# Kernel optimization log

Hardware: AMD Instinct MI355X
Metric: run time of the kernel (lower is better)

Reference implementation:

```python
import jax, jax.numpy as jnp
import numpy as np

B, S, D, H = 2, 2048, 1024, 16
DH = D // H  # 64


def setup_inputs() -> dict:
    key = jax.random.key(0)
    ks = jax.random.split(key, 6)
    scale = 1.0 / np.sqrt(D)
    x = jax.random.normal(ks[0], (B, S, D), dtype=jnp.float32)
    Wq = jax.random.normal(ks[1], (D, D), dtype=jnp.float32) * scale
    Wk = jax.random.normal(ks[2], (D, D), dtype=jnp.float32) * scale
    Wv = jax.random.normal(ks[3], (D, D), dtype=jnp.float32) * scale
    Wo = jax.random.normal(ks[4], (D, D), dtype=jnp.float32) * scale
    zeros = jnp.zeros((D,), dtype=jnp.float32)
    return {"x": x, "Wq": Wq, "bq": zeros, "Wk": Wk, "bk": zeros,
            "Wv": Wv, "bv": zeros, "Wo": Wo, "bo": zeros}


def reference(x, Wq, bq, Wk, bk, Wv, bv, Wo, bo):
    # x: [B, S, D]
    def split_heads(t):
        # [B, S, D] -> [B, H, S, DH]
        return t.reshape(B, S, H, DH).transpose(0, 2, 1, 3)

    q = split_heads(x @ Wq + bq)
    k = split_heads(x @ Wk + bk)
    v = split_heads(x @ Wv + bv)

    scores = jnp.einsum('bhqd,bhkd->bhqk', q, k) / jnp.sqrt(jnp.float32(DH))
    weights = jax.nn.softmax(scores, axis=-1)          # [B, H, S, S]
    o = jnp.einsum('bhqk,bhkd->bhqd', weights, v)       # [B, H, S, DH]
    o = o.transpose(0, 2, 1, 3).reshape(B, S, D)        # merge heads
    return o @ Wo + bo
```

## Files before the change

kernel.cpp:

```cpp
#include <hip/hip_runtime.h>
#include <hip/hip_bf16.h>

#define DEV __device__ __forceinline__

typedef short bf16x8 __attribute__((ext_vector_type(8)));
typedef float f32x4 __attribute__((ext_vector_type(4)));
typedef unsigned int u32;

constexpr int BB = 2, SS = 2048, DD = 1024, HH = 16, DHD = 64;
constexpr int MM = BB * SS;
#define QSC 0.1803368801111f

#if __has_builtin(__builtin_amdgcn_exp2f)
#define EXP2(x) __builtin_amdgcn_exp2f(x)
#else
#define EXP2(x) exp2f(x)
#endif

DEV unsigned short f2bf(float f) {
    union { float f; unsigned int u; } v; v.f = f;
    return (unsigned short)((v.u + 0x8000u) >> 16);
}
DEV u32 pk2bf(float a, float b) {
    union { float f; u32 u; } ua, ub; ua.f = a; ub.f = b;
    return ((ua.u + 0x8000u) >> 16) | ((ub.u + 0x8000u) & 0xffff0000u);
}

DEV bf16x8 ld_bf16x8(const unsigned short* p) { return *(const bf16x8*)p; }

DEV void gl16(const unsigned short* g, unsigned short* l) {
    __builtin_amdgcn_global_load_lds(
        (const __attribute__((address_space(1))) u32*)g,
        (__attribute__((address_space(3))) u32*)l, 16, 0, 0);
}

__global__ void x2bf(const float* __restrict__ x, unsigned short* __restrict__ xb) {
    int i = blockIdx.x * 256 + threadIdx.x;
    float4 v = ((const float4*)x)[i];
    uint2 o;
    o.x = pk2bf(v.x, v.y);
    o.y = pk2bf(v.z, v.w);
    ((uint2*)xb)[i] = o;
}

__global__ void transpose_w4(const float* __restrict__ W0, const float* __restrict__ W1,
                             const float* __restrict__ W2, const float* __restrict__ W3,
                             unsigned short* __restrict__ WtBase) {
    __shared__ float tile[32][33];
    const float* W = (blockIdx.z == 0) ? W0 : (blockIdx.z == 1) ? W1 : (blockIdx.z == 2) ? W2 : W3;
    unsigned short* Wt = WtBase + (size_t)blockIdx.z * DD * DD;
    int n0 = blockIdx.x * 32, k0 = blockIdx.y * 32;
    int tx = threadIdx.x, ty = threadIdx.y;
    #pragma unroll
    for (int i = 0; i < 4; ++i)
        tile[ty + 8 * i][tx] = W[(size_t)(k0 + ty + 8 * i) * DD + n0 + tx];
    __syncthreads();
    #pragma unroll
    for (int i = 0; i < 4; ++i)
        Wt[(size_t)(n0 + ty + 8 * i) * DD + k0 + tx] = f2bf(tile[tx][ty + 8 * i]);
}

__global__ __launch_bounds__(256) void qkv_gemm(
    const unsigned short* __restrict__ xb,
    const unsigned short* __restrict__ WtBase,
    const float* __restrict__ bq, const float* __restrict__ bk, const float* __restrict__ bv,
    unsigned short* __restrict__ Qb, unsigned short* __restrict__ Kb, unsigned short* __restrict__ Vt)
{
    __shared__ __align__(16) unsigned short Ald[2][128 * 32];
    __shared__ __align__(16) unsigned short Bld[2][128 * 32];

    const int z = blockIdx.z;
    const unsigned short* Wt = WtBase + (size_t)z * DD * DD;
    const float* bias = (z == 0) ? bq : (z == 1) ? bk : bv;

    const int m0g = blockIdx.y * 128;
    const int n0g = blockIdx.x * 128;
    const int wave = threadIdx.x >> 6, lane = threadIdx.x & 63;
    const int quad = lane >> 4, lcol = lane & 15;
    const int mb = (wave & 1) * 64, nb = (wave >> 1) * 64;

    f32x4 acc[4][4];
    #pragma unroll
    for (int i = 0; i < 4; ++i)
        #pragma unroll
        for (int j = 0; j < 4; ++j) acc[i][j] = (f32x4){0.f, 0.f, 0.f, 0.f};

    auto stage = [&](int ks, int bf) {
        #pragma unroll
        for (int i = 0; i < 4; ++i) {
            int j = wave * 4 + i;
            if (j < 8) {
                int bi = j * 64 + lane;
                int row = bi >> 2, p = (bi & 3) ^ (row & 3);
                gl16(xb + (size_t)(m0g + row) * DD + ks + p * 8, &Ald[bf][j * 512]);
            } else {
                int jj = j - 8;
                int bi = jj * 64 + lane;
                int row = bi >> 2, p = (bi & 3) ^ (row & 3);
                gl16(Wt + (size_t)(n0g + row) * DD + ks + p * 8, &Bld[bf][jj * 512]);
            }
        }
    };

    stage(0, 0);
    __syncthreads();

    for (int kk = 0; kk < 32; ++kk) {
        int bf = kk & 1;
        if (kk + 1 < 32) stage((kk + 1) * 32, (kk + 1) & 1);
        bf16x8 af[4], bfr[4];
        #pragma unroll
        for (int mt = 0; mt < 4; ++mt) {
            int row = mb + mt * 16 + lcol;
            af[mt] = ld_bf16x8(&Ald[bf][(row * 4 + (quad ^ (row & 3))) * 8]);
        }
        #pragma unroll
        for (int nt = 0; nt < 4; ++nt) {
            int row = nb + nt * 16 + lcol;
            bfr[nt] = ld_bf16x8(&Bld[bf][(row * 4 + (quad ^ (row & 3))) * 8]);
        }
        if (z < 2) {
            #pragma unroll
            for (int mt = 0; mt < 4; ++mt)
                #pragma unroll
                for (int nt = 0; nt < 4; ++nt)
                    acc[mt][nt] = __builtin_amdgcn_mfma_f32_16x16x32_bf16(bfr[nt], af[mt], acc[mt][nt], 0, 0, 0);
        } else {
            #pragma unroll
            for (int mt = 0; mt < 4; ++mt)
                #pragma unroll
                for (int nt = 0; nt < 4; ++nt)
                    acc[mt][nt] = __builtin_amdgcn_mfma_f32_16x16x32_bf16(af[mt], bfr[nt], acc[mt][nt], 0, 0, 0);
        }
        __syncthreads();
    }

    if (z < 2) {
        unsigned short* dst = (z == 0) ? Qb : Kb;
        const float sc = (z == 0) ? QSC : 1.0f;
        #pragma unroll
        for (int mt = 0; mt < 4; ++mt)
            #pragma unroll
            for (int nt = 0; nt < 4; ++nt) {
                int m = m0g + mb + mt * 16 + lcol;
                int nbt = n0g + nb + nt * 16 + quad * 4;
                int b = m >> 11, s = m & (SS - 1);
                int h = nbt >> 6, dh0 = nbt & 63;
                float4 bv4 = *(const float4*)&bias[nbt];
                uint2 o;
                o.x = pk2bf((acc[mt][nt][0] + bv4.x) * sc, (acc[mt][nt][1] + bv4.y) * sc);
                o.y = pk2bf((acc[mt][nt][2] + bv4.z) * sc, (acc[mt][nt][3] + bv4.w) * sc);
                *(uint2*)&dst[(((size_t)b * HH + h) * SS + s) * DHD + dh0] = o;
            }
    } else {
        #pragma unroll
        for (int mt = 0; mt < 4; ++mt)
            #pragma unroll
            for (int nt = 0; nt < 4; ++nt) {
                int n = n0g + nb + nt * 16 + lcol;
                int mbt = m0g + mb + mt * 16 + quad * 4;
                int h = n >> 6, dh = n & 63;
                int b = mbt >> 11, s0 = mbt & (SS - 1);
                float bvv = bias[n];
                uint2 o;
                o.x = pk2bf(acc[mt][nt][0] + bvv, acc[mt][nt][1] + bvv);
                o.y = pk2bf(acc[mt][nt][2] + bvv, acc[mt][nt][3] + bvv);
                *(uint2*)&Vt[(((size_t)b * HH + h) * DHD + dh) * SS + s0] = o;
            }
    }
}

__global__ __launch_bounds__(256) void attn(
    const unsigned short* __restrict__ Qb,
    const unsigned short* __restrict__ Kb,
    const unsigned short* __restrict__ Vt,
    unsigned short* __restrict__ Ob)
{
    __shared__ __align__(16) unsigned short Kld[2][64 * 64];
    __shared__ __align__(16) unsigned short Vld[2][64 * 64];
    __shared__ __align__(16) unsigned short tb[4][2][16 * 72];

    const int qt = blockIdx.x;
    const int bh = blockIdx.y;
    const int b = bh >> 4, h = bh & (HH - 1);
    const unsigned short* Qbh = Qb + (size_t)bh * SS * DHD;
    const unsigned short* Kbh = Kb + (size_t)bh * SS * DHD;
    const unsigned short* Vbh = Vt + (size_t)bh * DHD * SS;

    const int wave = threadIdx.x >> 6, lane = threadIdx.x & 63;
    const int quad = lane >> 4, lcol = lane & 15;
    const int rowbase = qt * 128 + wave * 32;

    bf16x8 qf[2][2];
    #pragma unroll
    for (int mt = 0; mt < 2; ++mt)
        #pragma unroll
        for (int kf = 0; kf < 2; ++kf)
            qf[mt][kf] = ld_bf16x8(Qbh + (size_t)(rowbase + mt * 16 + lcol) * DHD + kf * 32 + quad * 8);

    auto stage = [&](int c, int bf) {
        int kb = c * 64;
        #pragma unroll
        for (int i = 0; i < 4; ++i) {
            int j = wave * 4 + i;
            if (j < 8) {
                int bi = j * 64 + lane;
                int r = bi >> 3, p = (bi & 7) ^ (r & 7);
                gl16(Kbh + (size_t)(kb + r) * DHD + p * 8, &Kld[bf][j * 512]);
            } else {
                int jj = j - 8;
                int bi = jj * 64 + lane;
                int dh = bi >> 3, p = (bi & 7) ^ (dh & 7);
                gl16(Vbh + (size_t)dh * SS + kb + p * 8, &Vld[bf][jj * 512]);
            }
        }
    };

    stage(0, 0);
    __syncthreads();

    float m0 = -1e30f;
    #pragma unroll
    for (int kt = 0; kt < 4; ++kt) {
        int r0 = kt * 16 + lcol;
        bf16x8 ka0 = ld_bf16x8(&Kld[0][(r0 * 8 + (quad ^ (r0 & 7))) * 8]);
        bf16x8 ka1 = ld_bf16x8(&Kld[0][(r0 * 8 + ((quad + 4) ^ (r0 & 7))) * 8]);
        #pragma unroll
        for (int mt = 0; mt < 2; ++mt) {
            f32x4 s = (f32x4){0.f, 0.f, 0.f, 0.f};
            s = __builtin_amdgcn_mfma_f32_16x16x32_bf16(ka0, qf[mt][0], s, 0, 0, 0);
            s = __builtin_amdgcn_mfma_f32_16x16x32_bf16(ka1, qf[mt][1], s, 0, 0, 0);
            #pragma unroll
            for (int r = 0; r < 4; ++r) m0 = fmaxf(m0, s[r]);
        }
    }
    #pragma unroll
    for (int msk = 1; msk < 64; msk <<= 1) m0 = fmaxf(m0, __shfl_xor(m0, msk, 64));

    f32x4 oacc[2][4];
    #pragma unroll
    for (int mt = 0; mt < 2; ++mt)
        #pragma unroll
        for (int nt = 0; nt < 4; ++nt) oacc[mt][nt] = (f32x4){0.f, 0.f, 0.f, 0.f};
    float ps[2] = {0.f, 0.f};

    for (int c = 0; c < 32; ++c) {
        int bf = c & 1;
        if (c + 1 < 32) stage(c + 1, (c + 1) & 1);

        #pragma unroll
        for (int kt = 0; kt < 4; ++kt) {
            int r0 = kt * 16 + lcol;
            bf16x8 ka0 = ld_bf16x8(&Kld[bf][(r0 * 8 + (quad ^ (r0 & 7))) * 8]);
            bf16x8 ka1 = ld_bf16x8(&Kld[bf][(r0 * 8 + ((quad + 4) ^ (r0 & 7))) * 8]);
            #pragma unroll
            for (int mt = 0; mt < 2; ++mt) {
                f32x4 s = (f32x4){0.f, 0.f, 0.f, 0.f};
                s = __builtin_amdgcn_mfma_f32_16x16x32_bf16(ka0, qf[mt][0], s, 0, 0, 0);
                s = __builtin_amdgcn_mfma_f32_16x16x32_bf16(ka1, qf[mt][1], s, 0, 0, 0);
                float e0 = EXP2(s[0] - m0), e1 = EXP2(s[1] - m0);
                float e2 = EXP2(s[2] - m0), e3 = EXP2(s[3] - m0);
                ps[mt] += (e0 + e1) + (e2 + e3);
                *(uint2*)&tb[wave][mt][lcol * 72 + kt * 16 + quad * 4] =
                    make_uint2(pk2bf(e0, e1), pk2bf(e2, e3));
            }
        }

        #pragma unroll
        for (int kf2 = 0; kf2 < 2; ++kf2) {
            bf16x8 vb[4];
            #pragma unroll
            for (int nt = 0; nt < 4; ++nt) {
                int dh = nt * 16 + lcol;
                vb[nt] = ld_bf16x8(&Vld[bf][(dh * 8 + ((kf2 * 4 + quad) ^ (dh & 7))) * 8]);
            }
            #pragma unroll
            for (int mt = 0; mt < 2; ++mt) {
                bf16x8 pa = *(const bf16x8*)&tb[wave][mt][lcol * 72 + kf2 * 32 + quad * 8];
                #pragma unroll
                for (int nt = 0; nt < 4; ++nt)
                    oacc[mt][nt] = __builtin_amdgcn_mfma_f32_16x16x32_bf16(pa, vb[nt], oacc[mt][nt], 0, 0, 0);
            }
        }
        __syncthreads();
    }

    #pragma unroll
    for (int mt = 0; mt < 2; ++mt) {
        ps[mt] += __shfl_xor(ps[mt], 16, 64);
        ps[mt] += __shfl_xor(ps[mt], 32, 64);
    }
    float inv[2] = {1.0f / ps[0], 1.0f / ps[1]};
    #pragma unroll
    for (int mt = 0; mt < 2; ++mt)
        #pragma unroll
        for (int r = 0; r < 4; ++r) {
            float iv = __shfl(inv[mt], quad * 4 + r, 64);
            int srow = rowbase + mt * 16 + quad * 4 + r;
            size_t base = (((size_t)b * SS + srow) * HH + h) * DHD;
            #pragma unroll
            for (int nt = 0; nt < 4; ++nt)
                Ob[base + nt * 16 + lcol] = f2bf(oacc[mt][nt][r] * iv);
        }
}

__global__ __launch_bounds__(256) void out_gemm(
    const unsigned short* __restrict__ Ob,
    const unsigned short* __restrict__ Wto,
    const float* __restrict__ bo,
    float* __restrict__ out)
{
    __shared__ __align__(16) unsigned short Ald[2][128 * 32];
    __shared__ __align__(16) unsigned short Bld[2][128 * 32];

    const int m0g = blockIdx.y * 128;
    const int n0g = blockIdx.x * 128;
    const int wave = threadIdx.x >> 6, lane = threadIdx.x & 63;
    const int quad = lane >> 4, lcol = lane & 15;
    const int mb = (wave & 1) * 64, nb = (wave >> 1) * 64;

    f32x4 acc[4][4];
    #pragma unroll
    for (int i = 0; i < 4; ++i)
        #pragma unroll
        for (int j = 0; j < 4; ++j) acc[i][j] = (f32x4){0.f, 0.f, 0.f, 0.f};

    auto stage = [&](int ks, int bf) {
        #pragma unroll
        for (int i = 0; i < 4; ++i) {
            int j = wave * 4 + i;
            if (j < 8) {
                int bi = j * 64 + lane;
                int row = bi >> 2, p = (bi & 3) ^ (row & 3);
                gl16(Ob + (size_t)(m0g + row) * DD + ks + p * 8, &Ald[bf][j * 512]);
            } else {
                int jj = j - 8;
                int bi = jj * 64 + lane;
                int row = bi >> 2, p = (bi & 3) ^ (row & 3);
                gl16(Wto + (size_t)(n0g + row) * DD + ks + p * 8, &Bld[bf][jj * 512]);
            }
        }
    };

    stage(0, 0);
    __syncthreads();

    for (int kk = 0; kk < 32; ++kk) {
        int bf = kk & 1;
        if (kk + 1 < 32) stage((kk + 1) * 32, (kk + 1) & 1);
        bf16x8 af[4], bfr[4];
        #pragma unroll
        for (int mt = 0; mt < 4; ++mt) {
            int row = mb + mt * 16 + lcol;
            af[mt] = ld_bf16x8(&Ald[bf][(row * 4 + (quad ^ (row & 3))) * 8]);
        }
        #pragma unroll
        for (int nt = 0; nt < 4; ++nt) {
            int row = nb + nt * 16 + lcol;
            bfr[nt] = ld_bf16x8(&Bld[bf][(row * 4 + (quad ^ (row & 3))) * 8]);
        }
        #pragma unroll
        for (int mt = 0; mt < 4; ++mt)
            #pragma unroll
            for (int nt = 0; nt < 4; ++nt)
                acc[mt][nt] = __builtin_amdgcn_mfma_f32_16x16x32_bf16(af[mt], bfr[nt], acc[mt][nt], 0, 0, 0);
        __syncthreads();
    }

    #pragma unroll
    for (int mt = 0; mt < 4; ++mt)
        #pragma unroll
        for (int nt = 0; nt < 4; ++nt) {
            int n = n0g + nb + nt * 16 + lcol;
            float bv_ = bo[n];
            #pragma unroll
            for (int r = 0; r < 4; ++r) {
                int m = m0g + mb + mt * 16 + quad * 4 + r;
                out[(size_t)m * DD + n] = acc[mt][nt][r] + bv_;
            }
        }
}

extern "C" void kernel_launch(void* const* d_in, const int* in_sizes, int n_in,
                              void* d_out, int out_size, void* d_ws, size_t ws_size,
                              hipStream_t stream)
{
    const float* x  = (const float*)d_in[0];
    const float* Wq = (const float*)d_in[1];
    const float* bq = (const float*)d_in[2];
    const float* Wk = (const float*)d_in[3];
    const float* bk = (const float*)d_in[4];
    const float* Wv = (const float*)d_in[5];
    const float* bv = (const float*)d_in[6];
    const float* Wo = (const float*)d_in[7];
    const float* bo = (const float*)d_in[8];
    float* out = (float*)d_out;

    unsigned short* ws = (unsigned short*)d_ws;
    unsigned short* Wt  = ws;
    unsigned short* Wto = Wt + 3 * (size_t)DD * DD;
    unsigned short* Qb  = Wt + 4 * (size_t)DD * DD;
    unsigned short* Kb  = Qb + (size_t)MM * DD;
    unsigned short* Vt  = Kb + (size_t)MM * DD;
    unsigned short* xb  = Vt + (size_t)MM * DD;
    unsigned short* Ob  = xb;

    x2bf<<<MM * DD / 4 / 256, 256, 0, stream>>>(x, xb);
    transpose_w4<<<dim3(DD / 32, DD / 32, 4), dim3(32, 8), 0, stream>>>(Wq, Wk, Wv, Wo, Wt);

    qkv_gemm<<<dim3(DD / 128, MM / 128, 3), 256, 0, stream>>>(xb, Wt, bq, bk, bv, Qb, Kb, Vt);

    attn<<<dim3(SS / 128, BB * HH), 256, 0, stream>>>(Qb, Kb, Vt, Ob);

    out_gemm<<<dim3(DD / 128, MM / 128), 256, 0, stream>>>(Ob, Wto, bo, out);
}
```

Baseline: 221.4 us.

## Split attention keys across two waves with direct global loads and LDS merge

```diff
diff --git a/kernel.cpp b/kernel.cpp
--- a/kernel.cpp
+++ b/kernel.cpp
@@ -21,10 +21,17 @@
     union { float f; unsigned int u; } v; v.f = f;
     return (unsigned short)((v.u + 0x8000u) >> 16);
 }
+#if __has_builtin(__builtin_amdgcn_perm)
+DEV u32 pk2bf(float a, float b) {
+    union { float f; u32 u; } ua, ub; ua.f = a; ub.f = b;
+    return __builtin_amdgcn_perm(ub.u + 0x8000u, ua.u + 0x8000u, 0x07060302u);
+}
+#else
 DEV u32 pk2bf(float a, float b) {
     union { float f; u32 u; } ua, ub; ua.f = a; ub.f = b;
     return ((ua.u + 0x8000u) >> 16) | ((ub.u + 0x8000u) & 0xffff0000u);
 }
+#endif
 
 DEV bf16x8 ld_bf16x8(const unsigned short* p) { return *(const bf16x8*)p; }
 
@@ -170,18 +177,20 @@
     }
 }
 
-__global__ __launch_bounds__(256) void attn(
+__global__ __launch_bounds__(128) void attn(
     const unsigned short* __restrict__ Qb,
     const unsigned short* __restrict__ Kb,
     const unsigned short* __restrict__ Vt,
     unsigned short* __restrict__ Ob)
 {
-    __shared__ __align__(16) unsigned short Kld[2][64 * 64];
-    __shared__ __align__(16) unsigned short Vld[2][64 * 64];
-    __shared__ __align__(16) unsigned short tb[4][2][16 * 72];
-
-    const int qt = blockIdx.x;
-    const int bh = blockIdx.y;
+    __shared__ __align__(16) unsigned short tb[2][2][16 * 72];
+    __shared__ __align__(16) float Obuf[32][68];
+    __shared__ float lbuf[2][32];
+    __shared__ float mbuf[2];
+
+    const int g = blockIdx.y * gridDim.x + blockIdx.x;
+    const int bh = (g & 7) * 4 + ((g >> 3) & 3);
+    const int qt = g >> 5;
     const int b = bh >> 4, h = bh & (HH - 1);
     const unsigned short* Qbh = Qb + (size_t)bh * SS * DHD;
     const unsigned short* Kbh = Kb + (size_t)bh * SS * DHD;
@@ -189,7 +198,8 @@
 
     const int wave = threadIdx.x >> 6, lane = threadIdx.x & 63;
     const int quad = lane >> 4, lcol = lane & 15;
-    const int rowbase = qt * 128 + wave * 32;
+    const int rowbase = qt * 32;
+    const int key0 = wave * 1024;
 
     bf16x8 qf[2][2];
     #pragma unroll
@@ -198,33 +208,12 @@
         for (int kf = 0; kf < 2; ++kf)
             qf[mt][kf] = ld_bf16x8(Qbh + (size_t)(rowbase + mt * 16 + lcol) * DHD + kf * 32 + quad * 8);
 
-    auto stage = [&](int c, int bf) {
-        int kb = c * 64;
-        #pragma unroll
-        for (int i = 0; i < 4; ++i) {
-            int j = wave * 4 + i;
-            if (j < 8) {
-                int bi = j * 64 + lane;
-                int r = bi >> 3, p = (bi & 7) ^ (r & 7);
-                gl16(Kbh + (size_t)(kb + r) * DHD + p * 8, &Kld[bf][j * 512]);
-            } else {
-                int jj = j - 8;
-                int bi = jj * 64 + lane;
-                int dh = bi >> 3, p = (bi & 7) ^ (dh & 7);
-                gl16(Vbh + (size_t)dh * SS + kb + p * 8, &Vld[bf][jj * 512]);
-            }
-        }
-    };
-
-    stage(0, 0);
-    __syncthreads();
-
     float m0 = -1e30f;
     #pragma unroll
-    for (int kt = 0; kt < 4; ++kt) {
-        int r0 = kt * 16 + lcol;
-        bf16x8 ka0 = ld_bf16x8(&Kld[0][(r0 * 8 + (quad ^ (r0 & 7))) * 8]);
-        bf16x8 ka1 = ld_bf16x8(&Kld[0][(r0 * 8 + ((quad + 4) ^ (r0 & 7))) * 8]);
+    for (int kt = 0; kt < 2; ++kt) {
+        const unsigned short* kp = Kbh + (size_t)(key0 + kt * 16 + lcol) * DHD + quad * 8;
+        bf16x8 ka0 = ld_bf16x8(kp);
+        bf16x8 ka1 = ld_bf16x8(kp + 32);
         #pragma unroll
         for (int mt = 0; mt < 2; ++mt) {
             f32x4 s = (f32x4){0.f, 0.f, 0.f, 0.f};
@@ -236,6 +225,7 @@
     }
     #pragma unroll
     for (int msk = 1; msk < 64; msk <<= 1) m0 = fmaxf(m0, __shfl_xor(m0, msk, 64));
+    const f32x4 minit = (f32x4){-m0, -m0, -m0, -m0};
 
     f32x4 oacc[2][4];
     #pragma unroll
@@ -244,22 +234,21 @@
         for (int nt = 0; nt < 4; ++nt) oacc[mt][nt] = (f32x4){0.f, 0.f, 0.f, 0.f};
     float ps[2] = {0.f, 0.f};
 
-    for (int c = 0; c < 32; ++c) {
-        int bf = c & 1;
-        if (c + 1 < 32) stage(c + 1, (c + 1) & 1);
+    for (int c = 0; c < 16; ++c) {
+        const int kb = key0 + c * 64;
 
         #pragma unroll
         for (int kt = 0; kt < 4; ++kt) {
-            int r0 = kt * 16 + lcol;
-            bf16x8 ka0 = ld_bf16x8(&Kld[bf][(r0 * 8 + (quad ^ (r0 & 7))) * 8]);
-            bf16x8 ka1 = ld_bf16x8(&Kld[bf][(r0 * 8 + ((quad + 4) ^ (r0 & 7))) * 8]);
+            const unsigned short* kp = Kbh + (size_t)(kb + kt * 16 + lcol) * DHD + quad * 8;
+            bf16x8 ka0 = ld_bf16x8(kp);
+            bf16x8 ka1 = ld_bf16x8(kp + 32);
             #pragma unroll
             for (int mt = 0; mt < 2; ++mt) {
-                f32x4 s = (f32x4){0.f, 0.f, 0.f, 0.f};
+                f32x4 s = minit;
                 s = __builtin_amdgcn_mfma_f32_16x16x32_bf16(ka0, qf[mt][0], s, 0, 0, 0);
                 s = __builtin_amdgcn_mfma_f32_16x16x32_bf16(ka1, qf[mt][1], s, 0, 0, 0);
-                float e0 = EXP2(s[0] - m0), e1 = EXP2(s[1] - m0);
-                float e2 = EXP2(s[2] - m0), e3 = EXP2(s[3] - m0);
+                float e0 = EXP2(s[0]), e1 = EXP2(s[1]);
+                float e2 = EXP2(s[2]), e3 = EXP2(s[3]);
                 ps[mt] += (e0 + e1) + (e2 + e3);
                 *(uint2*)&tb[wave][mt][lcol * 72 + kt * 16 + quad * 4] =
                     make_uint2(pk2bf(e0, e1), pk2bf(e2, e3));
@@ -270,10 +259,8 @@
         for (int kf2 = 0; kf2 < 2; ++kf2) {
             bf16x8 vb[4];
             #pragma unroll
-            for (int nt = 0; nt < 4; ++nt) {
-                int dh = nt * 16 + lcol;
-                vb[nt] = ld_bf16x8(&Vld[bf][(dh * 8 + ((kf2 * 4 + quad) ^ (dh & 7))) * 8]);
-            }
+            for (int nt = 0; nt < 4; ++nt)
+                vb[nt] = ld_bf16x8(Vbh + (size_t)(nt * 16 + lcol) * SS + kb + kf2 * 32 + quad * 8);
             #pragma unroll
             for (int mt = 0; mt < 2; ++mt) {
                 bf16x8 pa = *(const bf16x8*)&tb[wave][mt][lcol * 72 + kf2 * 32 + quad * 8];
@@ -282,7 +269,6 @@
                     oacc[mt][nt] = __builtin_amdgcn_mfma_f32_16x16x32_bf16(pa, vb[nt], oacc[mt][nt], 0, 0, 0);
             }
         }
-        __syncthreads();
     }
 
     #pragma unroll
@@ -290,18 +276,57 @@
         ps[mt] += __shfl_xor(ps[mt], 16, 64);
         ps[mt] += __shfl_xor(ps[mt], 32, 64);
     }
-    float inv[2] = {1.0f / ps[0], 1.0f / ps[1]};
-    #pragma unroll
-    for (int mt = 0; mt < 2; ++mt)
-        #pragma unroll
-        for (int r = 0; r < 4; ++r) {
-            float iv = __shfl(inv[mt], quad * 4 + r, 64);
-            int srow = rowbase + mt * 16 + quad * 4 + r;
-            size_t base = (((size_t)b * SS + srow) * HH + h) * DHD;
+
+    if (lane == 0) mbuf[wave] = m0;
+    __syncthreads();
+    const float M = fmaxf(mbuf[0], mbuf[1]);
+    const float alpha = EXP2(m0 - M);
+
+    if (quad == 0) {
+        #pragma unroll
+        for (int mt = 0; mt < 2; ++mt)
+            lbuf[wave][mt * 16 + lcol] = alpha * ps[mt];
+    }
+    if (wave == 0) {
+        #pragma unroll
+        for (int mt = 0; mt < 2; ++mt)
             #pragma unroll
             for (int nt = 0; nt < 4; ++nt)
-                Ob[base + nt * 16 + lcol] = f2bf(oacc[mt][nt][r] * iv);
-        }
+                #pragma unroll
+                for (int r = 0; r < 4; ++r)
+                    Obuf[mt * 16 + quad * 4 + r][nt * 16 + lcol] = alpha * oacc[mt][nt][r];
+    }
+    __syncthreads();
+    if (wave == 1) {
+        #pragma unroll
+        for (int mt = 0; mt < 2; ++mt)
+            #pragma unroll
+            for (int nt = 0; nt < 4; ++nt)
+                #pragma unroll
+                for (int r = 0; r < 4; ++r)
+                    Obuf[mt * 16 + quad * 4 + r][nt * 16 + lcol] += alpha * oacc[mt][nt][r];
+    }
+    __syncthreads();
+
+    {
+        const int t = threadIdx.x;
+        const int row = t >> 2;
+        const int dh0 = (t & 3) * 16;
+        float inv = 1.0f / (lbuf[0][row] + lbuf[1][row]);
+        const float* src = &Obuf[row][dh0];
+        uint4 o0, o1;
+        o0.x = pk2bf(src[0] * inv,  src[1] * inv);
+        o0.y = pk2bf(src[2] * inv,  src[3] * inv);
+        o0.z = pk2bf(src[4] * inv,  src[5] * inv);
+        o0.w = pk2bf(src[6] * inv,  src[7] * inv);
+        o1.x = pk2bf(src[8] * inv,  src[9] * inv);
+        o1.y = pk2bf(src[10] * inv, src[11] * inv);
+        o1.z = pk2bf(src[12] * inv, src[13] * inv);
+        o1.w = pk2bf(src[14] * inv, src[15] * inv);
+        size_t base = (((size_t)b * SS + rowbase + row) * HH + h) * DHD + dh0;
+        *(uint4*)&Ob[base] = o0;
+        *(uint4*)&Ob[base + 8] = o1;
+    }
 }
 
 __global__ __launch_bounds__(256) void out_gemm(
@@ -310,31 +335,31 @@
     const float* __restrict__ bo,
     float* __restrict__ out)
 {
-    __shared__ __align__(16) unsigned short Ald[2][128 * 32];
+    __shared__ __align__(16) unsigned short Ald[2][64 * 32];
     __shared__ __align__(16) unsigned short Bld[2][128 * 32];
 
-    const int m0g = blockIdx.y * 128;
+    const int m0g = blockIdx.y * 64;
     const int n0g = blockIdx.x * 128;
     const int wave = threadIdx.x >> 6, lane = threadIdx.x & 63;
     const int quad = lane >> 4, lcol = lane & 15;
-    const int mb = (wave & 1) * 64, nb = (wave >> 1) * 64;
-
-    f32x4 acc[4][4];
+    const int nb = wave * 32;
+
+    f32x4 acc[4][2];
     #pragma unroll
     for (int i = 0; i < 4; ++i)
         #pragma unroll
-        for (int j = 0; j < 4; ++j) acc[i][j] = (f32x4){0.f, 0.f, 0.f, 0.f};
+        for (int j = 0; j < 2; ++j) acc[i][j] = (f32x4){0.f, 0.f, 0.f, 0.f};
 
     auto stage = [&](int ks, int bf) {
         #pragma unroll
-        for (int i = 0; i < 4; ++i) {
-            int j = wave * 4 + i;
-            if (j < 8) {
+        for (int i = 0; i < 3; ++i) {
+            int j = wave * 3 + i;
+            if (j < 4) {
                 int bi = j * 64 + lane;
                 int row = bi >> 2, p = (bi & 3) ^ (row & 3);
                 gl16(Ob + (size_t)(m0g + row) * DD + ks + p * 8, &Ald[bf][j * 512]);
             } else {
-                int jj = j - 8;
+                int jj = j - 4;
                 int bi = jj * 64 + lane;
                 int row = bi >> 2, p = (bi & 3) ^ (row & 3);
                 gl16(Wto + (size_t)(n0g + row) * DD + ks + p * 8, &Bld[bf][jj * 512]);
@@ -348,21 +373,21 @@
     for (int kk = 0; kk < 32; ++kk) {
         int bf = kk & 1;
         if (kk + 1 < 32) stage((kk + 1) * 32, (kk + 1) & 1);
-        bf16x8 af[4], bfr[4];
+        bf16x8 af[4], bfr[2];
         #pragma unroll
         for (int mt = 0; mt < 4; ++mt) {
-            int row = mb + mt * 16 + lcol;
+            int row = mt * 16 + lcol;
             af[mt] = ld_bf16x8(&Ald[bf][(row * 4 + (quad ^ (row & 3))) * 8]);
         }
         #pragma unroll
-        for (int nt = 0; nt < 4; ++nt) {
+        for (int nt = 0; nt < 2; ++nt) {
             int row = nb + nt * 16 + lcol;
             bfr[nt] = ld_bf16x8(&Bld[bf][(row * 4 + (quad ^ (row & 3))) * 8]);
         }
         #pragma unroll
         for (int mt = 0; mt < 4; ++mt)
             #pragma unroll
-            for (int nt = 0; nt < 4; ++nt)
+            for (int nt = 0; nt < 2; ++nt)
                 acc[mt][nt] = __builtin_amdgcn_mfma_f32_16x16x32_bf16(af[mt], bfr[nt], acc[mt][nt], 0, 0, 0);
         __syncthreads();
     }
@@ -370,12 +395,12 @@
     #pragma unroll
     for (int mt = 0; mt < 4; ++mt)
         #pragma unroll
-        for (int nt = 0; nt < 4; ++nt) {
+        for (int nt = 0; nt < 2; ++nt) {
             int n = n0g + nb + nt * 16 + lcol;
             float bv_ = bo[n];
             #pragma unroll
             for (int r = 0; r < 4; ++r) {
-                int m = m0g + mb + mt * 16 + quad * 4 + r;
+                int m = m0g + mt * 16 + quad * 4 + r;
                 out[(size_t)m * DD + n] = acc[mt][nt][r] + bv_;
             }
         }
@@ -410,7 +435,7 @@
 
     qkv_gemm<<<dim3(DD / 128, MM / 128, 3), 256, 0, stream>>>(xb, Wt, bq, bk, bv, Qb, Kb, Vt);
 
-    attn<<<dim3(SS / 128, BB * HH), 256, 0, stream>>>(Qb, Kb, Vt, Ob);
-
-    out_gemm<<<dim3(DD / 128, MM / 128), 256, 0, stream>>>(Ob, Wto, bo, out);
-}
+    attn<<<dim3(64, 32), 128, 0, stream>>>(Qb, Kb, Vt, Ob);
+
+    out_gemm<<<dim3(DD / 128, MM / 64), 256, 0, stream>>>(Ob, Wto, bo, out);
+}
```

Measured after the change: 282.7 us. 27.7% more time.
